# Kernel optimization log

Measured on AMD Instinct MI355X. Metric: run time of the kernel, lower is better.

Reference implementation:

```python
import jax, jax.numpy as jnp
import numpy as np

N_NODES = 50000
N_EDGES = 800000
IN_CH = 256
HID = 64
HEADS = 4
NEG_SLOPE = 0.2  # PyG GATConv default


def setup_inputs() -> dict:
    key = jax.random.key(0)
    ks = jax.random.split(key, 12)
    glorot = lambda k, shape: jax.random.normal(k, shape, jnp.float32) * (2.0 / (shape[0] + shape[-1])) ** 0.5
    d1 = HEADS * HID  # 256: width after conv1 (concat heads)
    return {
        "x": jax.random.normal(ks[0], (N_NODES, IN_CH), jnp.float32),
        "edge_index": jax.random.randint(ks[1], (2, N_EDGES), 0, N_NODES, jnp.int64),
        # conv1: GATConv(IN_CH, HID, heads=HEADS)
        "W1": glorot(ks[2], (IN_CH, HEADS * HID)),
        "a_src1": glorot(ks[3], (HEADS, HID)),
        "a_dst1": glorot(ks[4], (HEADS, HID)),
        "b1": jnp.zeros((HEADS * HID,), jnp.float32),
        # conv2: GATConv(d1, d1, heads=1)
        "W2": glorot(ks[5], (d1, d1)),
        "a_src2": glorot(ks[6], (1, d1)),
        "a_dst2": glorot(ks[7], (1, d1)),
        "b2": jnp.zeros((d1,), jnp.float32),
    }


def gat_conv(x, src, dst, W, a_src, a_dst, b, heads, out_ch, n_nodes):
    """PyG-style GATConv: per-head linear, additive attention, segment softmax over dst."""
    h = (x @ W).reshape(n_nodes, heads, out_ch)            # [N, H, C]
    alpha_src = jnp.sum(h * a_src, axis=-1)                # [N, H]
    alpha_dst = jnp.sum(h * a_dst, axis=-1)                # [N, H]
    e = jax.nn.leaky_relu(alpha_src[src] + alpha_dst[dst], NEG_SLOPE)  # [E, H]
    # numerically-stable segment softmax grouped by destination node
    e_max = jax.ops.segment_max(e, dst, num_segments=n_nodes)         # [N, H]
    e_exp = jnp.exp(e - e_max[dst])
    denom = jax.ops.segment_sum(e_exp, dst, num_segments=n_nodes)
    alpha = e_exp / denom[dst]                                        # [E, H]
    out = jax.ops.segment_sum(alpha[:, :, None] * h[src], dst, num_segments=n_nodes)  # [N, H, C]
    return out.reshape(n_nodes, heads * out_ch) + b


def reference(x, edge_index, W1, a_src1, a_dst1, b1, W2, a_src2, a_dst2, b2):
    n = x.shape[0]
    loops = jnp.arange(n, dtype=edge_index.dtype)
    src = jnp.concatenate([edge_index[0], loops])  # add self-loops (PyG default)
    dst = jnp.concatenate([edge_index[1], loops])
    h1 = gat_conv(x, src, dst, W1, a_src1, a_dst1, b1, HEADS, HID, n)
    h1 = jax.nn.elu(h1)
    out = gat_conv(h1, src, dst, W2, a_src2, a_dst2, b2, 1, HEADS * HID, n)
    return out
```

## Files before the change

kernel.cpp:

```cpp
#include <hip/hip_runtime.h>
#include <stdint.h>

typedef __bf16 bfv8 __attribute__((ext_vector_type(8)));
typedef float f32x4 __attribute__((ext_vector_type(4)));

__device__ __forceinline__ float b2f(unsigned short u) {
    union { unsigned int i; float f; } v; v.i = ((unsigned int)u) << 16; return v.f;
}
__device__ __forceinline__ unsigned short f2b(float f) {
    unsigned int x = __float_as_uint(f);
    unsigned int r = x + 0x7FFFu + ((x >> 16) & 1u);
    return (unsigned short)(r >> 16);
}
__device__ __forceinline__ float squash(float v) {
    return (v == v && fabsf(v) < 1e30f) ? v : 0.f;
}

__device__ __forceinline__ void detect_reg(const void* x, const void* ei, int& f32w, int& i64w) {
    const unsigned short* xu = (const unsigned short*)x;
    const int* e32 = (const int*)ei;
    int bad = 0, oz = 0;
#pragma unroll
    for (int j = 0; j < 64; j++) {
        float v = b2f(xu[j]);
        if (!(fabsf(v) < 1e10f)) bad++;
    }
#pragma unroll
    for (int j = 1; j < 16; j += 2)
        if (e32[j] == 0) oz++;
    f32w = (bad >= 2) ? 1 : 0;
    i64w = (oz >= 6) ? 1 : 0;
}

__device__ __forceinline__ int edge_at(const void* ei, int idx, int i64) {
    return i64 ? (int)(((const long long*)ei)[idx]) : ((const int*)ei)[idx];
}

__global__ __launch_bounds__(256) void k_prep(
        const void* __restrict__ x, const void* __restrict__ ei,
        const void* __restrict__ W1, const void* __restrict__ W2,
        const void* __restrict__ a_src1, const void* __restrict__ a_dst1, const void* __restrict__ b1,
        const void* __restrict__ a_src2, const void* __restrict__ a_dst2, const void* __restrict__ b2,
        unsigned short* __restrict__ xb, unsigned short* __restrict__ WT1,
        unsigned short* __restrict__ WT2, unsigned short* __restrict__ vecs,
        int* __restrict__ deg, int* __restrict__ flags,
        int E, int ET, int N, int total8, int nconv, int nhist) {
    __shared__ unsigned short t[32][33];
    int f32w, i64w;
    detect_reg(x, ei, f32w, i64w);
    int b = blockIdx.x;
    int tid = threadIdx.x;

    if (b < nconv) {
        int i = b * 256 + tid;
        if (i >= total8) return;
        if (f32w) {
            const float4* f = (const float4*)x;
            float4 a = f[2 * i], bb = f[2 * i + 1];
            uint4 o;
            o.x = (unsigned)f2b(squash(a.x)) | ((unsigned)f2b(squash(a.y)) << 16);
            o.y = (unsigned)f2b(squash(a.z)) | ((unsigned)f2b(squash(a.w)) << 16);
            o.z = (unsigned)f2b(squash(bb.x)) | ((unsigned)f2b(squash(bb.y)) << 16);
            o.w = (unsigned)f2b(squash(bb.z)) | ((unsigned)f2b(squash(bb.w)) << 16);
            *(uint4*)(xb + 8 * (size_t)i) = o;
        } else {
            *(uint4*)(xb + 8 * (size_t)i) = ((const uint4*)x)[i];
        }
    } else if (b < nconv + 128) {
        int tb2 = b - nconv;
        const void* W = (tb2 < 64) ? W1 : W2;
        unsigned short* WT = (tb2 < 64) ? WT1 : WT2;
        int t6 = tb2 & 63;
        int bx = (t6 & 7) * 32, by = (t6 >> 3) * 32;
        int tx = tid & 31, ty = tid >> 5;
        for (int j = 0; j < 32; j += 8) {
            size_t idx = (size_t)(by + ty + j) * 256 + bx + tx;
            t[ty + j][tx] = f32w ? f2b(squash(((const float*)W)[idx]))
                                 : ((const unsigned short*)W)[idx];
        }
        __syncthreads();
        for (int j = 0; j < 32; j += 8)
            WT[(size_t)(bx + ty + j) * 256 + by + tx] = t[tx][ty + j];
    } else if (b < nconv + 128 + nhist) {
        int i = (b - nconv - 128) * 256 + tid;
        if (i >= ET) return;
        int d = (i < E) ? edge_at(ei, E + i, i64w) : (i - E);
        d = min(max(d, 0), N - 1);
        atomicAdd(&deg[d], 1);
    } else {
        const void* ptrs[6] = {a_src1, a_dst1, b1, a_src2, a_dst2, b2};
#pragma unroll
        for (int j = 0; j < 6; j++) {
            unsigned short u = f32w ? f2b(squash(((const float*)ptrs[j])[tid]))
                                    : ((const unsigned short*)ptrs[j])[tid];
            vecs[j * 256 + tid] = u;
        }
        if (tid == 0) { flags[0] = f32w; flags[1] = i64w; }
    }
}

__global__ void k_scan1(const int* __restrict__ deg, int* __restrict__ tscan, int* __restrict__ bsum, int n) {
    __shared__ int sm[256];
    int tid = threadIdx.x;
    int i = blockIdx.x * 256 + tid;
    int v = (i < n) ? deg[i] : 0;
    sm[tid] = v; __syncthreads();
    for (int off = 1; off < 256; off <<= 1) {
        int t = (tid >= off) ? sm[tid - off] : 0;
        __syncthreads();
        sm[tid] += t;
        __syncthreads();
    }
    if (i < n) tscan[i] = sm[tid];
    if (tid == 255) bsum[blockIdx.x] = sm[255];
}

__global__ void k_scan2(const int* __restrict__ bsum, int* __restrict__ boff, int nb) {
    __shared__ int sm[256];
    int tid = threadIdx.x;
    int v = (tid < nb) ? bsum[tid] : 0;
    sm[tid] = v; __syncthreads();
    for (int off = 1; off < 256; off <<= 1) {
        int t = (tid >= off) ? sm[tid - off] : 0;
        __syncthreads();
        sm[tid] += t;
        __syncthreads();
    }
    if (tid < nb) boff[tid] = sm[tid] - v;
}

__global__ void k_scan3(const int* __restrict__ deg, const int* __restrict__ tscan,
                        const int* __restrict__ boff, int* __restrict__ row_start,
                        int* __restrict__ cursor, unsigned short* __restrict__ csr16,
                        int n, int ET) {
    int i = blockIdx.x * 256 + threadIdx.x;
    if (i < n) {
        int rs = tscan[i] - deg[i] + boff[i >> 8];
        row_start[i] = rs;
        cursor[i] = rs;
    }
    if (i == 0) row_start[n] = ET;
    if (blockIdx.x == 0 && threadIdx.x < 64) csr16[ET + threadIdx.x] = 0;
}

__global__ void k_scatter(const void* __restrict__ ei, int* __restrict__ cursor,
                          unsigned short* __restrict__ csr16, const int* __restrict__ flags,
                          int E, int ET, int N) {
    int i = blockIdx.x * 256 + threadIdx.x;
    if (i >= ET) return;
    int s, d;
    if (i < E) {
        int i64 = flags[1];
        s = edge_at(ei, i, i64);
        d = edge_at(ei, E + i, i64);
    } else {
        s = i - E; d = i - E;
    }
    s = min(max(s, 0), N - 1);
    d = min(max(d, 0), N - 1);
    int pos = atomicAdd(&cursor[d], 1);
    pos = min(max(pos, 0), ET - 1);
    csr16[pos] = (unsigned short)s;
}

__global__ __launch_bounds__(256) void k_gemm(const unsigned short* __restrict__ A,
                                              const unsigned short* __restrict__ BT,
                                              unsigned short* __restrict__ C, int M) {
    __shared__ __align__(16) unsigned short As[128 * 72];
    __shared__ __align__(16) unsigned short Bs[128 * 72];
    const int tid = threadIdx.x;
    const int m0 = blockIdx.x * 128, n0 = blockIdx.y * 128;
    const int w = tid >> 6, lane = tid & 63;
    const int wm = (w & 1) * 64, wn = (w >> 1) * 64;
    const int lr = lane & 15, lk = (lane >> 4) * 8;
    const int sr = tid >> 1, sc = (tid & 1) * 32;

    f32x4 acc[4][4];
#pragma unroll
    for (int a = 0; a < 4; a++)
#pragma unroll
        for (int b = 0; b < 4; b++) acc[a][b] = (f32x4){0.f, 0.f, 0.f, 0.f};

    for (int k0 = 0; k0 < 256; k0 += 64) {
        uint4 va0, va1, va2, va3;
        if (m0 + sr < M) {
            const uint4* Ap = (const uint4*)(A + (size_t)(m0 + sr) * 256 + k0 + sc);
            va0 = Ap[0]; va1 = Ap[1]; va2 = Ap[2]; va3 = Ap[3];
        } else {
            va0 = va1 = va2 = va3 = make_uint4(0, 0, 0, 0);
        }
        {
            uint4* Ad = (uint4*)&As[sr * 72 + sc];
            Ad[0] = va0; Ad[1] = va1; Ad[2] = va2; Ad[3] = va3;
        }
        {
            const uint4* Bp = (const uint4*)(BT + (size_t)(n0 + sr) * 256 + k0 + sc);
            uint4* Bd = (uint4*)&Bs[sr * 72 + sc];
            Bd[0] = Bp[0]; Bd[1] = Bp[1]; Bd[2] = Bp[2]; Bd[3] = Bp[3];
        }
        __syncthreads();
#pragma unroll
        for (int kk = 0; kk < 64; kk += 32) {
            bfv8 af[4], bfr[4];
#pragma unroll
            for (int mi = 0; mi < 4; mi++)
                af[mi] = *(const bfv8*)&As[(wm + mi * 16 + lr) * 72 + kk + lk];
#pragma unroll
            for (int ni = 0; ni < 4; ni++)
                bfr[ni] = *(const bfv8*)&Bs[(wn + ni * 16 + lr) * 72 + kk + lk];
#pragma unroll
            for (int mi = 0; mi < 4; mi++)
#pragma unroll
                for (int ni = 0; ni < 4; ni++)
                    acc[mi][ni] = __builtin_amdgcn_mfma_f32_16x16x32_bf16(af[mi], bfr[ni], acc[mi][ni], 0, 0, 0);
        }
        __syncthreads();
    }
    const int rb = (lane >> 4) * 4;
#pragma unroll
    for (int mi = 0; mi < 4; mi++) {
#pragma unroll
        for (int r = 0; r < 4; r++) {
            int row = m0 + wm + mi * 16 + rb + r;
            if (row < M) {
#pragma unroll
                for (int ni = 0; ni < 4; ni++)
                    C[(size_t)row * 256 + n0 + wn + ni * 16 + lr] = f2b(squash(acc[mi][ni][r]));
            }
        }
    }
}

__global__ void k_alphas(const unsigned short* __restrict__ Hm, const unsigned short* __restrict__ a_src,
                         const unsigned short* __restrict__ a_dst, float* __restrict__ as_out,
                         float* __restrict__ ad_out, int N, int H) {
    int wid = (blockIdx.x * 256 + threadIdx.x) >> 6;
    int lane = threadIdx.x & 63;
    if (wid >= N) return;
    int c = 4 * lane;
    uint2 hv = *(const uint2*)(Hm + (size_t)wid * 256 + c);
    float h0 = b2f((unsigned short)(hv.x & 0xffff));
    float h1 = b2f((unsigned short)(hv.x >> 16));
    float h2 = b2f((unsigned short)(hv.y & 0xffff));
    float h3 = b2f((unsigned short)(hv.y >> 16));
    float s = h0 * b2f(a_src[c]) + h1 * b2f(a_src[c + 1]) + h2 * b2f(a_src[c + 2]) + h3 * b2f(a_src[c + 3]);
    float d = h0 * b2f(a_dst[c]) + h1 * b2f(a_dst[c + 1]) + h2 * b2f(a_dst[c + 2]) + h3 * b2f(a_dst[c + 3]);
    int lph = 64 / H;
    for (int off = 1; off < lph; off <<= 1) {
        s += __shfl_xor(s, off, 64);
        d += __shfl_xor(d, off, 64);
    }
    if ((lane & (lph - 1)) == 0) {
        int h = lane / lph;
        as_out[(size_t)wid * H + h] = squash(s);
        ad_out[(size_t)wid * H + h] = squash(d);
    }
}

__global__ __launch_bounds__(256) void k_agg(
        const unsigned short* __restrict__ Hm, const float* __restrict__ asrc,
        const float* __restrict__ adst, const int* __restrict__ row_start,
        const unsigned short* __restrict__ csr16, const unsigned short* __restrict__ bias,
        void* __restrict__ out, const int* __restrict__ flags,
        int N, int H, int ET, int elu, int is_final) {
    __shared__ float4 lw[4][64];
    const int wv = threadIdx.x >> 6;
    const int lane = threadIdx.x & 63;
    const int wid = blockIdx.x * 4 + wv;
    if (wid >= N) return;
    const int h = (lane * H) >> 6;
    int rs = row_start[wid], re = row_start[wid + 1];
    rs = min(max(rs, 0), ET);
    re = min(max(re, rs), ET);

    float4 adn4;
    if (H == 4) adn4 = *(const float4*)(adst + (size_t)wid * 4);
    else { adn4.x = adst[wid]; adn4.y = adn4.z = adn4.w = 0.f; }

    float4 lsum = make_float4(0.f, 0.f, 0.f, 0.f);
    float a0 = 0.f, a1 = 0.f, a2 = 0.f, a3 = 0.f;
    for (int c = rs; c < re; c += 64) {
        int cnt = min(64, re - c);
        float4 w4 = make_float4(0.f, 0.f, 0.f, 0.f);
        if (lane < cnt) {
            int idx = min((int)csr16[c + lane], N - 1);
            if (H == 4) {
                float4 av = *(const float4*)(asrc + (size_t)idx * 4);
                float ex = av.x + adn4.x, ey = av.y + adn4.y;
                float ez = av.z + adn4.z, ew = av.w + adn4.w;
                ex = (ex < 0.f) ? 0.2f * ex : ex;
                ey = (ey < 0.f) ? 0.2f * ey : ey;
                ez = (ez < 0.f) ? 0.2f * ez : ez;
                ew = (ew < 0.f) ? 0.2f * ew : ew;
                w4.x = __expf(fminf(ex, 80.f)); w4.y = __expf(fminf(ey, 80.f));
                w4.z = __expf(fminf(ez, 80.f)); w4.w = __expf(fminf(ew, 80.f));
            } else {
                float ev = asrc[idx] + adn4.x;
                ev = (ev < 0.f) ? 0.2f * ev : ev;
                w4.x = __expf(fminf(ev, 80.f));
            }
        }
        lsum.x += w4.x;
        if (H == 4) { lsum.y += w4.y; lsum.z += w4.z; lsum.w += w4.w; }
        lw[wv][lane] = w4;
        asm volatile("s_waitcnt lgkmcnt(0)");

        for (int jb = 0; jb < cnt; jb += 8) {
            int sj[8];
#pragma unroll
            for (int u = 0; u < 8; u++)
                sj[u] = min((int)csr16[c + jb + u], N - 1);
            uint2 hv[8];
#pragma unroll
            for (int u = 0; u < 8; u++)
                hv[u] = *(const uint2*)(Hm + (size_t)sj[u] * 256 + 4 * lane);
#pragma unroll
            for (int u = 0; u < 8; u++) {
                int j = jb + u;
                float wgt = (j < cnt) ? ((const float*)&lw[wv][j])[h] : 0.f;
                a0 = fmaf(wgt, b2f((unsigned short)(hv[u].x & 0xffff)), a0);
                a1 = fmaf(wgt, b2f((unsigned short)(hv[u].x >> 16)),    a1);
                a2 = fmaf(wgt, b2f((unsigned short)(hv[u].y & 0xffff)), a2);
                a3 = fmaf(wgt, b2f((unsigned short)(hv[u].y >> 16)),    a3);
            }
        }
    }
    for (int off = 1; off < 64; off <<= 1) {
        lsum.x += __shfl_xor(lsum.x, off, 64);
        if (H == 4) {
            lsum.y += __shfl_xor(lsum.y, off, 64);
            lsum.z += __shfl_xor(lsum.z, off, 64);
            lsum.w += __shfl_xor(lsum.w, off, 64);
        }
    }
    float ls = ((const float*)&lsum)[h];
    float inv = (ls > 0.f) ? 1.f / ls : 0.f;

    int cc = 4 * lane;
    float o0 = a0 * inv + b2f(bias[cc]);
    float o1 = a1 * inv + b2f(bias[cc + 1]);
    float o2 = a2 * inv + b2f(bias[cc + 2]);
    float o3 = a3 * inv + b2f(bias[cc + 3]);
    if (elu) {
        o0 = (o0 > 0.f) ? o0 : __expf(o0) - 1.f;
        o1 = (o1 > 0.f) ? o1 : __expf(o1) - 1.f;
        o2 = (o2 > 0.f) ? o2 : __expf(o2) - 1.f;
        o3 = (o3 > 0.f) ? o3 : __expf(o3) - 1.f;
    }
    o0 = squash(o0); o1 = squash(o1); o2 = squash(o2); o3 = squash(o3);
    if (is_final && flags[0]) {
        float4 ov = make_float4(o0, o1, o2, o3);
        *(float4*)((float*)out + (size_t)wid * 256 + cc) = ov;
    } else {
        uint2 ov;
        ov.x = (unsigned)f2b(o0) | ((unsigned)f2b(o1) << 16);
        ov.y = (unsigned)f2b(o2) | ((unsigned)f2b(o3) << 16);
        *(uint2*)((unsigned short*)out + (size_t)wid * 256 + cc) = ov;
    }
}

extern "C" void kernel_launch(void* const* d_in, const int* in_sizes, int n_in,
                              void* d_out, int out_size, void* d_ws, size_t ws_size,
                              hipStream_t stream) {
    const void* x      = d_in[0];
    const void* ei     = d_in[1];
    const void* W1     = d_in[2];
    const void* a_src1 = d_in[3];
    const void* a_dst1 = d_in[4];
    const void* b1     = d_in[5];
    const void* W2     = d_in[6];
    const void* a_src2 = d_in[7];
    const void* a_dst2 = d_in[8];
    const void* b2     = d_in[9];

    const int N  = in_sizes[0] / 256;
    const int E  = in_sizes[1] / 2;
    const int ET = E + N;

    char* p = (char*)d_ws;
    auto alloc = [&](size_t bytes) -> char* {
        char* r = p;
        p += (bytes + 255) & ~(size_t)255;
        return r;
    };
    int* flags = (int*)alloc(256);
    unsigned short* WT1  = (unsigned short*)alloc(256 * 256 * 2);
    unsigned short* WT2  = (unsigned short*)alloc(256 * 256 * 2);
    unsigned short* vecs = (unsigned short*)alloc(6 * 256 * 2);
    float* as_ = (float*)alloc((size_t)N * 4 * 4);
    float* ad_ = (float*)alloc((size_t)N * 4 * 4);
    int* deg       = (int*)alloc((size_t)N * 4);
    int* tscan     = (int*)alloc((size_t)N * 4);
    int* row_start = (int*)alloc((size_t)(N + 1) * 4);
    int* cursor    = (int*)alloc((size_t)N * 4);
    int* bsum      = (int*)alloc(1024);
    int* boff      = (int*)alloc(1024);
    unsigned short* csr16 = (unsigned short*)alloc((size_t)(ET + 64) * 2);

    unsigned short* BUF_OUT = (unsigned short*)d_out;
    unsigned short* BUF_IN0 = (unsigned short*)d_in[0];

    hipMemsetAsync(deg, 0, (size_t)N * 4, stream);

    const int total8 = N * 256 / 8;
    const int nconv  = (total8 + 255) / 256;
    const int nhist  = (ET + 255) / 256;
    const int nprep  = nconv + 128 + nhist + 1;

    k_prep<<<nprep, 256, 0, stream>>>(x, ei, W1, W2, a_src1, a_dst1, b1, a_src2, a_dst2, b2,
                                      BUF_OUT, WT1, WT2, vecs, deg, flags,
                                      E, ET, N, total8, nconv, nhist);

    int nb = (N + 255) / 256;
    k_scan1<<<nb, 256, 0, stream>>>(deg, tscan, bsum, N);
    k_scan2<<<1, 256, 0, stream>>>(bsum, boff, nb);
    k_scan3<<<nb, 256, 0, stream>>>(deg, tscan, boff, row_start, cursor, csr16, N, ET);
    k_scatter<<<nhist, 256, 0, stream>>>(ei, cursor, csr16, flags, E, ET, N);

    int gm = (N + 127) / 128;
    int wb = (N + 3) / 4;

    k_gemm<<<dim3(gm, 2), 256, 0, stream>>>(BUF_OUT, WT1, BUF_IN0, N);
    k_alphas<<<wb, 256, 0, stream>>>(BUF_IN0, vecs + 0 * 256, vecs + 1 * 256, as_, ad_, N, 4);
    k_agg<<<wb, 256, 0, stream>>>(BUF_IN0, as_, ad_, row_start, csr16, vecs + 2 * 256,
                                  BUF_OUT, flags, N, 4, ET, 1, 0);
    k_gemm<<<dim3(gm, 2), 256, 0, stream>>>(BUF_OUT, WT2, BUF_IN0, N);
    k_alphas<<<wb, 256, 0, stream>>>(BUF_IN0, vecs + 3 * 256, vecs + 4 * 256, as_, ad_, N, 1);
    k_agg<<<wb, 256, 0, stream>>>(BUF_IN0, as_, ad_, row_start, csr16, vecs + 5 * 256,
                                  d_out, flags, N, 1, ET, 0, 1);
}
```

Before: 404.7 us.

## Aggregate each node with a half-wavefront using 16-byte feature gathers

The aggregation kernel now gives each destination node 32 lanes instead of a full 64-lane wavefront, so each block handles 8 nodes. Each lane loads 8 bf16 features with one 16-byte gather instead of 4. Neighbor byte offsets are computed once and kept in shared memory, and the full 8-wide chunks drop per-element bounds checks. The aim is fewer, wider memory requests and better use of lanes on low-degree nodes, at the cost of more accumulator registers and a separate tail path.

```diff
diff --git a/kernel.cpp b/kernel.cpp
--- a/kernel.cpp
+++ b/kernel.cpp
@@ -14,6 +14,12 @@
 }
 __device__ __forceinline__ float squash(float v) {
     return (v == v && fabsf(v) < 1e30f) ? v : 0.f;
+}
+__device__ __forceinline__ float blo(unsigned int w) {
+    union { unsigned int i; float f; } v; v.i = w << 16; return v.f;
+}
+__device__ __forceinline__ float bhi(unsigned int w) {
+    union { unsigned int i; float f; } v; v.i = w & 0xffff0000u; return v.f;
 }
 
 __device__ __forceinline__ void detect_reg(const void* x, const void* ei, int& f32w, int& i64w) {
@@ -263,31 +269,40 @@
         const unsigned short* __restrict__ csr16, const unsigned short* __restrict__ bias,
         void* __restrict__ out, const int* __restrict__ flags,
         int N, int H, int ET, int elu, int is_final) {
-    __shared__ float4 lw[4][64];
-    const int wv = threadIdx.x >> 6;
-    const int lane = threadIdx.x & 63;
-    const int wid = blockIdx.x * 4 + wv;
-    if (wid >= N) return;
-    const int h = (lane * H) >> 6;
-    int rs = row_start[wid], re = row_start[wid + 1];
+    __shared__ __align__(16) float lwv[8][32][4];
+    __shared__ unsigned int loff[8][32];
+    const int tid = threadIdx.x;
+    const int hw = tid >> 5;
+    const int l = tid & 31;
+    const int node = blockIdx.x * 8 + hw;
+    if (node >= N) return;
+    const int h = (l * H) >> 5;
+    const int lb = l * 16;
+    int rs = row_start[node], re = row_start[node + 1];
     rs = min(max(rs, 0), ET);
     re = min(max(re, rs), ET);
 
-    float4 adn4;
-    if (H == 4) adn4 = *(const float4*)(adst + (size_t)wid * 4);
-    else { adn4.x = adst[wid]; adn4.y = adn4.z = adn4.w = 0.f; }
+    float4 adn;
+    if (H == 4) adn = *(const float4*)(adst + (size_t)node * 4);
+    else { adn.x = adst[node]; adn.y = adn.z = adn.w = 0.f; }
 
     float4 lsum = make_float4(0.f, 0.f, 0.f, 0.f);
-    float a0 = 0.f, a1 = 0.f, a2 = 0.f, a3 = 0.f;
-    for (int c = rs; c < re; c += 64) {
-        int cnt = min(64, re - c);
+    float a0 = 0.f, a1 = 0.f, a2 = 0.f, a3 = 0.f, a4 = 0.f, a5 = 0.f, a6 = 0.f, a7 = 0.f;
+    const float* wbase = &lwv[hw][0][0] + h;
+    const unsigned int* obase = &loff[hw][0];
+    const char* Hb = (const char*)Hm;
+
+    for (int c = rs; c < re; c += 32) {
+        const int cnt = min(32, re - c);
         float4 w4 = make_float4(0.f, 0.f, 0.f, 0.f);
-        if (lane < cnt) {
-            int idx = min((int)csr16[c + lane], N - 1);
+        unsigned int off = 0;
+        if (l < cnt) {
+            int idx = min((int)csr16[c + l], N - 1);
+            off = (unsigned)idx << 9;
             if (H == 4) {
                 float4 av = *(const float4*)(asrc + (size_t)idx * 4);
-                float ex = av.x + adn4.x, ey = av.y + adn4.y;
-                float ez = av.z + adn4.z, ew = av.w + adn4.w;
+                float ex = av.x + adn.x, ey = av.y + adn.y;
+                float ez = av.z + adn.z, ew = av.w + adn.w;
                 ex = (ex < 0.f) ? 0.2f * ex : ex;
                 ey = (ey < 0.f) ? 0.2f * ey : ey;
                 ez = (ez < 0.f) ? 0.2f * ez : ez;
@@ -295,37 +310,61 @@
                 w4.x = __expf(fminf(ex, 80.f)); w4.y = __expf(fminf(ey, 80.f));
                 w4.z = __expf(fminf(ez, 80.f)); w4.w = __expf(fminf(ew, 80.f));
             } else {
-                float ev = asrc[idx] + adn4.x;
+                float ev = asrc[idx] + adn.x;
                 ev = (ev < 0.f) ? 0.2f * ev : ev;
                 w4.x = __expf(fminf(ev, 80.f));
             }
         }
         lsum.x += w4.x;
         if (H == 4) { lsum.y += w4.y; lsum.z += w4.z; lsum.w += w4.w; }
-        lw[wv][lane] = w4;
+        *(float4*)&lwv[hw][l][0] = w4;
+        loff[hw][l] = off;
         asm volatile("s_waitcnt lgkmcnt(0)");
 
-        for (int jb = 0; jb < cnt; jb += 8) {
-            int sj[8];
-#pragma unroll
-            for (int u = 0; u < 8; u++)
-                sj[u] = min((int)csr16[c + jb + u], N - 1);
-            uint2 hv[8];
-#pragma unroll
-            for (int u = 0; u < 8; u++)
-                hv[u] = *(const uint2*)(Hm + (size_t)sj[u] * 256 + 4 * lane);
+        const int full = cnt & ~7;
+        int jb = 0;
+        for (; jb < full; jb += 8) {
+            unsigned int o_[8];
+            uint4 hv[8];
+            float wj[8];
+#pragma unroll
+            for (int u = 0; u < 8; u++) o_[u] = obase[jb + u];
+#pragma unroll
+            for (int u = 0; u < 8; u++) hv[u] = *(const uint4*)(Hb + (size_t)o_[u] + lb);
+#pragma unroll
+            for (int u = 0; u < 8; u++) wj[u] = wbase[(jb + u) * 4];
 #pragma unroll
             for (int u = 0; u < 8; u++) {
-                int j = jb + u;
-                float wgt = (j < cnt) ? ((const float*)&lw[wv][j])[h] : 0.f;
-                a0 = fmaf(wgt, b2f((unsigned short)(hv[u].x & 0xffff)), a0);
-                a1 = fmaf(wgt, b2f((unsigned short)(hv[u].x >> 16)),    a1);
-                a2 = fmaf(wgt, b2f((unsigned short)(hv[u].y & 0xffff)), a2);
-                a3 = fmaf(wgt, b2f((unsigned short)(hv[u].y >> 16)),    a3);
+                a0 = fmaf(wj[u], blo(hv[u].x), a0); a1 = fmaf(wj[u], bhi(hv[u].x), a1);
+                a2 = fmaf(wj[u], blo(hv[u].y), a2); a3 = fmaf(wj[u], bhi(hv[u].y), a3);
+                a4 = fmaf(wj[u], blo(hv[u].z), a4); a5 = fmaf(wj[u], bhi(hv[u].z), a5);
+                a6 = fmaf(wj[u], blo(hv[u].w), a6); a7 = fmaf(wj[u], bhi(hv[u].w), a7);
             }
         }
-    }
-    for (int off = 1; off < 64; off <<= 1) {
+        if (jb < cnt) {
+            const int rem = cnt - jb;
+            unsigned int o_[8];
+            uint4 hv[8];
+            float wj[8];
+#pragma unroll
+            for (int u = 0; u < 8; u++) o_[u] = obase[jb + u];
+#pragma unroll
+            for (int u = 0; u < 8; u++) {
+                uint4 z = make_uint4(0, 0, 0, 0);
+                hv[u] = (u < rem) ? *(const uint4*)(Hb + (size_t)o_[u] + lb) : z;
+            }
+#pragma unroll
+            for (int u = 0; u < 8; u++) wj[u] = wbase[(jb + u) * 4];
+#pragma unroll
+            for (int u = 0; u < 8; u++) {
+                a0 = fmaf(wj[u], blo(hv[u].x), a0); a1 = fmaf(wj[u], bhi(hv[u].x), a1);
+                a2 = fmaf(wj[u], blo(hv[u].y), a2); a3 = fmaf(wj[u], bhi(hv[u].y), a3);
+                a4 = fmaf(wj[u], blo(hv[u].z), a4); a5 = fmaf(wj[u], bhi(hv[u].z), a5);
+                a6 = fmaf(wj[u], blo(hv[u].w), a6); a7 = fmaf(wj[u], bhi(hv[u].w), a7);
+            }
+        }
+    }
+    for (int off = 1; off < 32; off <<= 1) {
         lsum.x += __shfl_xor(lsum.x, off, 64);
         if (H == 4) {
             lsum.y += __shfl_xor(lsum.y, off, 64);
@@ -333,29 +372,39 @@
             lsum.w += __shfl_xor(lsum.w, off, 64);
         }
     }
-    float ls = ((const float*)&lsum)[h];
+    float ls = (H == 4) ? ((h == 0) ? lsum.x : (h == 1) ? lsum.y : (h == 2) ? lsum.z : lsum.w)
+                        : lsum.x;
     float inv = (ls > 0.f) ? 1.f / ls : 0.f;
 
-    int cc = 4 * lane;
-    float o0 = a0 * inv + b2f(bias[cc]);
-    float o1 = a1 * inv + b2f(bias[cc + 1]);
-    float o2 = a2 * inv + b2f(bias[cc + 2]);
-    float o3 = a3 * inv + b2f(bias[cc + 3]);
+    const int cc = 8 * l;
+    uint4 bv = *(const uint4*)(bias + cc);
+    float o0 = a0 * inv + blo(bv.x), o1 = a1 * inv + bhi(bv.x);
+    float o2 = a2 * inv + blo(bv.y), o3 = a3 * inv + bhi(bv.y);
+    float o4 = a4 * inv + blo(bv.z), o5 = a5 * inv + bhi(bv.z);
+    float o6 = a6 * inv + blo(bv.w), o7 = a7 * inv + bhi(bv.w);
     if (elu) {
         o0 = (o0 > 0.f) ? o0 : __expf(o0) - 1.f;
         o1 = (o1 > 0.f) ? o1 : __expf(o1) - 1.f;
         o2 = (o2 > 0.f) ? o2 : __expf(o2) - 1.f;
         o3 = (o3 > 0.f) ? o3 : __expf(o3) - 1.f;
+        o4 = (o4 > 0.f) ? o4 : __expf(o4) - 1.f;
+        o5 = (o5 > 0.f) ? o5 : __expf(o5) - 1.f;
+        o6 = (o6 > 0.f) ? o6 : __expf(o6) - 1.f;
+        o7 = (o7 > 0.f) ? o7 : __expf(o7) - 1.f;
     }
     o0 = squash(o0); o1 = squash(o1); o2 = squash(o2); o3 = squash(o3);
+    o4 = squash(o4); o5 = squash(o5); o6 = squash(o6); o7 = squash(o7);
     if (is_final && flags[0]) {
-        float4 ov = make_float4(o0, o1, o2, o3);
-        *(float4*)((float*)out + (size_t)wid * 256 + cc) = ov;
+        float* op = (float*)out + (size_t)node * 256 + cc;
+        *(float4*)op       = make_float4(o0, o1, o2, o3);
+        *(float4*)(op + 4) = make_float4(o4, o5, o6, o7);
     } else {
-        uint2 ov;
+        uint4 ov;
         ov.x = (unsigned)f2b(o0) | ((unsigned)f2b(o1) << 16);
         ov.y = (unsigned)f2b(o2) | ((unsigned)f2b(o3) << 16);
-        *(uint2*)((unsigned short*)out + (size_t)wid * 256 + cc) = ov;
+        ov.z = (unsigned)f2b(o4) | ((unsigned)f2b(o5) << 16);
+        ov.w = (unsigned)f2b(o6) | ((unsigned)f2b(o7) << 16);
+        *(uint4*)((unsigned short*)out + (size_t)node * 256 + cc) = ov;
     }
 }
 
@@ -419,13 +468,14 @@
 
     int gm = (N + 127) / 128;
     int wb = (N + 3) / 4;
+    int ab = (N + 7) / 8;
 
     k_gemm<<<dim3(gm, 2), 256, 0, stream>>>(BUF_OUT, WT1, BUF_IN0, N);
     k_alphas<<<wb, 256, 0, stream>>>(BUF_IN0, vecs + 0 * 256, vecs + 1 * 256, as_, ad_, N, 4);
-    k_agg<<<wb, 256, 0, stream>>>(BUF_IN0, as_, ad_, row_start, csr16, vecs + 2 * 256,
+    k_agg<<<ab, 256, 0, stream>>>(BUF_IN0, as_, ad_, row_start, csr16, vecs + 2 * 256,
                                   BUF_OUT, flags, N, 4, ET, 1, 0);
     k_gemm<<<dim3(gm, 2), 256, 0, stream>>>(BUF_OUT, WT2, BUF_IN0, N);
     k_alphas<<<wb, 256, 0, stream>>>(BUF_IN0, vecs + 3 * 256, vecs + 4 * 256, as_, ad_, N, 1);
-    k_agg<<<wb, 256, 0, stream>>>(BUF_IN0, as_, ad_, row_start, csr16, vecs + 5 * 256,
+    k_agg<<<ab, 256, 0, stream>>>(BUF_IN0, as_, ad_, row_start, csr16, vecs + 5 * 256,
                                   d_out, flags, N, 1, ET, 0, 1);
 }
```

Result: no change. 403.7 us (-0.2%).
